# Performance work log

Hardware: AMD Instinct MI355X
Metric: run time of the kernel (lower is better)

## Reference

```python
import jax, jax.numpy as jnp
import numpy as np

S = 128           # seq_len
B = 256           # input_bits (bits per token, also neurons per head)
H = 16            # num_heads
NB = 12           # n_bits_per_neuron -> LUT size 2^12
PB = 7            # relative-position bits = ceil(log2(max_seq_len))
HEAD_IN = 2 * B + PB   # concat(query, key, rel_pos_bits) = 519
THRESH = H // 2


def setup_inputs() -> dict:
    key = jax.random.key(0)
    k1, k2, k3 = jax.random.split(key, 3)
    tokens = jax.random.randint(k1, (S, B), 0, 2, dtype=jnp.int32)           # binary token bits
    memory = jax.random.normal(k2, (H, B, 2 ** NB), dtype=jnp.float32)       # RAM LUT contents per head/neuron
    connections = jax.random.randint(k3, (H, B, NB), 0, HEAD_IN, dtype=jnp.int32)  # per-neuron input-bit wiring
    return {"tokens": tokens, "memory": memory, "connections": connections}


def reference(tokens, memory, connections):
    idx = jnp.arange(S)
    rel = idx[:, None] - idx[None, :]                         # [S,S] i - j
    mask = (rel >= 0).astype(jnp.int32)                        # causal mask (j <= i)
    relc = jnp.clip(rel, 0, S - 1)
    # relative-distance binary encoding, LSB first: [S,S,PB]
    pos_bits = ((relc[..., None] >> jnp.arange(PB)) & 1).astype(jnp.int32)
    q = jnp.broadcast_to(tokens[:, None, :], (S, S, B))
    k = jnp.broadcast_to(tokens[None, :, :], (S, S, B))
    head_in = jnp.concatenate([q, k, pos_bits], axis=-1)       # [S,S,HEAD_IN]
    # RAM address per (query i, key j, head h, neuron n): pack NB wired bits, LSB first
    addr = jnp.zeros((S, S, H, B), dtype=jnp.int32)
    for b in range(NB):  # tiny fixed loop over bit planes, fully vectorized over S,S,H,B
        addr = addr + (head_in[..., connections[:, :, b]] << b)
    # LUT gather: memory[h, n, addr] -> [S,S,H,B]
    h_idx = jnp.arange(H)[:, None]
    n_idx = jnp.arange(B)[None, :]
    vals = memory[h_idx, n_idx, addr]
    bits = (vals > 0.0).astype(jnp.int32)                      # RAM neuron output bit
    # XOR accumulation over attended keys == masked sum mod 2: [S,H,B]
    head_res = jnp.sum(bits * mask[:, :, None, None], axis=1) % 2
    # majority vote across heads per bit
    ones_count = jnp.sum(head_res, axis=1)                     # [S,B]
    return (ones_count > THRESH).astype(jnp.int32)
```

## Files before the change

### kernel.cpp

```cpp
#include <hip/hip_runtime.h>


#define S 128
#define B 256
#define H 16
#define NB 12

__device__ __forceinline__ unsigned sig(unsigned x) {
    return x ^ ((x >> 3) & 0x70u) ^ ((x >> 6) & 0x70u);
}

__global__ __launch_bounds__(1024, 4) void softram_kernel(
    const int* __restrict__ tokens,
    const float* __restrict__ memory,
    const int* __restrict__ connections,
    int* __restrict__ out)
{
    const int n    = blockIdx.x;
    const int tid  = threadIdx.x;
    const int h    = tid >> 6;
    const int lane = tid & 63;

    __shared__ unsigned char  bytetab[H * 4096];
    __shared__ unsigned int   tokT[8][S];
    __shared__ unsigned short akT[H][S];
    __shared__ unsigned short apt[H][S];
    __shared__ int            conns[H][NB];
    __shared__ unsigned int   parts[H][4];

    const float4* mrow = (const float4*)(memory + ((size_t)(h * 256 + n) << 12));
    float4 va[16];
    #pragma unroll
    for (int t = 0; t < 16; ++t) va[t] = mrow[lane + 64 * t];

    {
        int i = tid >> 3, w = tid & 7;
        const int4* tp = (const int4*)tokens;
        unsigned v = 0;
        #pragma unroll
        for (int u = 0; u < 8; ++u) {
            int4 x = tp[i * 64 + w * 8 + u];
            v |= (unsigned)(x.x & 1) << (4 * u + 0);
            v |= (unsigned)(x.y & 1) << (4 * u + 1);
            v |= (unsigned)(x.z & 1) << (4 * u + 2);
            v |= (unsigned)(x.w & 1) << (4 * u + 3);
        }
        tokT[w][i] = v;
    }
    if (tid < H * NB) {
        int hh = tid / NB, b = tid - hh * NB;
        conns[hh][b] = connections[hh * (B * NB) + n * NB + b];
    }
    __syncthreads();

    unsigned qmask = 0, kmask = 0, pmask = 0;
    #pragma unroll
    for (int b = 0; b < NB; ++b) {
        int c = conns[h][b];
        qmask |= (unsigned)(c < 256) << b;
        kmask |= (unsigned)(c >= 256 && c < 512) << b;
        pmask |= (unsigned)(c >= 512) << b;
    }
    const int qb = __popc(qmask);
    const int kb = __popc(kmask);

    unsigned char* __restrict__ bt = &bytetab[h << 12];
    unsigned long long rlo = 0, rhi = 0;

    if (pmask == 0) {
        unsigned qcls0 = 0, qcls1 = 0;
        #pragma unroll
        for (int e = 0; e < 2; ++e) {
            int ii = lane + 64 * e;
            unsigned qc = 0, kc = 0;
            int qn = 0, kn = 0;
            #pragma unroll
            for (int b = 0; b < NB; ++b) {
                int c = conns[h][b];
                if (c < 256) {
                    qc |= ((tokT[c >> 5][ii] >> (c & 31)) & 1u) << qn;
                    ++qn;
                } else {
                    int c2 = c - 256;
                    kc |= ((tokT[c2 >> 5][ii] >> (c2 & 31)) & 1u) << kn;
                    ++kn;
                }
            }
            akT[h][ii] = (unsigned short)kc;
            if (e == 0) qcls0 = qc; else qcls1 = qc;
        }

        #pragma unroll
        for (int t = 0; t < 16; ++t) {
            float4 v = va[t];
            unsigned p = 4u * (unsigned)(lane + 64 * t);
            unsigned w = (unsigned)(v.x > 0.f)
                       | ((unsigned)(v.y > 0.f) << 8)
                       | ((unsigned)(v.z > 0.f) << 16)
                       | ((unsigned)(v.w > 0.f) << 24);
            *(unsigned*)&bt[sig(p)] = w;
        }

        const bool formA = (qb <= 6);
        const int SBITS  = formA ? qb : kb;
        unsigned apl = 0, aul = 0;
        {
            int scnt = 0, lcnt = 0;
            #pragma unroll
            for (int b = 0; b < NB; ++b) {
                int c = conns[h][b];
                bool isS = formA ? (c < 256) : (c >= 256);
                if (isS) {
                    apl |= (((unsigned)lane >> scnt) & 1u) << b;
                    ++scnt;
                } else {
                    int p = SBITS + lcnt;
                    if (p < 6) apl |= (((unsigned)lane >> p) & 1u) << b;
                    else       aul |= (((unsigned)lane >> (p - 6)) & 1u) << b;
                    ++lcnt;
                }
            }
        }
        const unsigned spl  = sig(apl);
        const unsigned saul = sig(aul);
        unsigned Wlo = 0, Whi = 0;
        #pragma unroll 8
        for (int it = 0; it < 64; ++it) {
            unsigned sau  = (unsigned)__builtin_amdgcn_readlane((int)saul, it);
            unsigned bitv = bt[sau ^ spl] & 1u;
            unsigned long long Bm = __ballot(bitv != 0u);
            Wlo = (lane == it) ? (unsigned)Bm : Wlo;
            Whi = (lane == it) ? (unsigned)(Bm >> 32) : Whi;
        }

        if (formA) {
            unsigned long long A = 0, cap0 = 0, cap1 = 0;
            for (int s8 = 0; s8 < 8; ++s8) {
                uint4 uk = *(const uint4*)&akT[h][s8 * 8];
                #pragma unroll
                for (int t = 0; t < 8; ++t) {
                    int j = s8 * 8 + t;
                    unsigned w = ((const unsigned*)&uk)[t >> 1];
                    unsigned widx = (unsigned)__builtin_amdgcn_readfirstlane(
                        (int)((w >> ((t & 1) * 16)) & 0xffffu));
                    unsigned g0 = widx << qb;
                    int lsel = (int)(g0 >> 6);
                    unsigned lo = (unsigned)__builtin_amdgcn_readlane((int)Wlo, lsel);
                    unsigned hi = (unsigned)__builtin_amdgcn_readlane((int)Whi, lsel);
                    A ^= ((((unsigned long long)hi << 32) | lo) >> (g0 & 63u));
                    cap0 = (lane == j) ? A : cap0;
                }
            }
            for (int s8 = 8; s8 < 16; ++s8) {
                uint4 uk = *(const uint4*)&akT[h][s8 * 8];
                #pragma unroll
                for (int t = 0; t < 8; ++t) {
                    int j = s8 * 8 + t;
                    unsigned w = ((const unsigned*)&uk)[t >> 1];
                    unsigned widx = (unsigned)__builtin_amdgcn_readfirstlane(
                        (int)((w >> ((t & 1) * 16)) & 0xffffu));
                    unsigned g0 = widx << qb;
                    int lsel = (int)(g0 >> 6);
                    unsigned lo = (unsigned)__builtin_amdgcn_readlane((int)Wlo, lsel);
                    unsigned hi = (unsigned)__builtin_amdgcn_readlane((int)Whi, lsel);
                    A ^= ((((unsigned long long)hi << 32) | lo) >> (g0 & 63u));
                    cap1 = (lane == j - 64) ? A : cap1;
                }
            }
            rlo = __ballot(((cap0 >> qcls0) & 1ull) != 0ull);
            rhi = __ballot(((cap1 >> qcls1) & 1ull) != 0ull);
        } else {
            unsigned Cw = 0, cap0 = 0, cap1 = 0;
            for (int s8 = 0; s8 < 8; ++s8) {
                uint4 uk = *(const uint4*)&akT[h][s8 * 8];
                #pragma unroll
                for (int t = 0; t < 8; ++t) {
                    int j = s8 * 8 + t;
                    unsigned w = ((const unsigned*)&uk)[t >> 1];
                    unsigned widx = (unsigned)__builtin_amdgcn_readfirstlane(
                        (int)((w >> ((t & 1) * 16)) & 0xffffu));
                    Cw ^= 1u << widx;
                    cap0 = (lane == j) ? Cw : cap0;
                }
            }
            for (int s8 = 8; s8 < 16; ++s8) {
                uint4 uk = *(const uint4*)&akT[h][s8 * 8];
                #pragma unroll
                for (int t = 0; t < 8; ++t) {
                    int j = s8 * 8 + t;
                    unsigned w = ((const unsigned*)&uk)[t >> 1];
                    unsigned widx = (unsigned)__builtin_amdgcn_readfirstlane(
                        (int)((w >> ((t & 1) * 16)) & 0xffffu));
                    Cw ^= 1u << widx;
                    cap1 = (lane == j - 64) ? Cw : cap1;
                }
            }
            unsigned g0a = qcls0 << kb, g0b = qcls1 << kb;
            unsigned lo0 = (unsigned)__shfl((int)Wlo, (int)(g0a >> 6));
            unsigned hi0 = (unsigned)__shfl((int)Whi, (int)(g0a >> 6));
            unsigned lo1 = (unsigned)__shfl((int)Wlo, (int)(g0b >> 6));
            unsigned hi1 = (unsigned)__shfl((int)Whi, (int)(g0b >> 6));
            unsigned W0 = (unsigned)((((unsigned long long)hi0 << 32) | lo0) >> (g0a & 63u));
            unsigned W1 = (unsigned)((((unsigned long long)hi1 << 32) | lo1) >> (g0b & 63u));
            rlo = __ballot((__popc(W0 & cap0) & 1) != 0);
            rhi = __ballot((__popc(W1 & cap1) & 1) != 0);
        }
    } else {
        unsigned aqv0 = 0, aqv1 = 0;
        #pragma unroll
        for (int e = 0; e < 2; ++e) {
            int ii = lane + 64 * e;
            unsigned aq = 0, ak = 0, ap = 0;
            #pragma unroll
            for (int b = 0; b < NB; ++b) {
                int c = conns[h][b];
                if (c < 256) {
                    aq |= ((tokT[c >> 5][ii] >> (c & 31)) & 1u) << b;
                } else if (c < 512) {
                    int c2 = c - 256;
                    ak |= ((tokT[c2 >> 5][ii] >> (c2 & 31)) & 1u) << b;
                } else {
                    ap |= (((unsigned)ii >> (c - 512)) & 1u) << b;
                }
            }
            akT[h][ii] = (unsigned short)sig(ak);
            apt[h][ii] = (unsigned short)sig(ap);
            if (e == 0) aqv0 = sig(aq); else aqv1 = sig(aq);
        }

        #pragma unroll
        for (int t = 0; t < 16; ++t) {
            float4 v = va[t];
            unsigned p = 4u * (unsigned)(lane + 64 * t);
            unsigned w = (unsigned)(v.x > 0.f)
                       | ((unsigned)(v.y > 0.f) << 8)
                       | ((unsigned)(v.z > 0.f) << 16)
                       | ((unsigned)(v.w > 0.f) << 24);
            *(unsigned*)&bt[sig(p)] = w;
        }

        unsigned acc0 = 0, acc1 = 0;
        for (int s8 = 0; s8 < 8; ++s8) {
            uint4 uk = *(const uint4*)&akT[h][s8 * 8];
            #pragma unroll
            for (int t = 0; t < 8; ++t) {
                int j = s8 * 8 + t;
                unsigned w = ((const unsigned*)&uk)[t >> 1];
                unsigned akv = (w >> ((t & 1) * 16)) & 0xffffu;
                int d0 = lane - j;
                unsigned v0 = bt[aqv0 ^ akv ^ (unsigned)apt[h][d0 & 127]] & 1u;
                acc0 ^= (d0 >= 0) ? v0 : 0u;
                int d1 = lane + 64 - j;
                unsigned v1 = bt[aqv1 ^ akv ^ (unsigned)apt[h][d1]] & 1u;
                acc1 ^= v1;
            }
        }
        for (int s8 = 8; s8 < 16; ++s8) {
            uint4 uk = *(const uint4*)&akT[h][s8 * 8];
            #pragma unroll
            for (int t = 0; t < 8; ++t) {
                int j = s8 * 8 + t;
                unsigned w = ((const unsigned*)&uk)[t >> 1];
                unsigned akv = (w >> ((t & 1) * 16)) & 0xffffu;
                int d1 = lane + 64 - j;
                unsigned v1 = bt[aqv1 ^ akv ^ (unsigned)apt[h][d1 & 127]] & 1u;
                acc1 ^= (d1 >= 0) ? v1 : 0u;
            }
        }
        rlo = __ballot(acc0 != 0u);
        rhi = __ballot(acc1 != 0u);
    }

    if (lane == 0) {
        parts[h][0] = (unsigned)rlo;
        parts[h][1] = (unsigned)(rlo >> 32);
        parts[h][2] = (unsigned)rhi;
        parts[h][3] = (unsigned)(rhi >> 32);
    }
    __syncthreads();

    if (tid < S) {
        int i = tid, tot = 0;
        #pragma unroll
        for (int hh = 0; hh < H; ++hh)
            tot += (parts[hh][i >> 5] >> (i & 31)) & 1;
        out[i * B + n] = (tot > (H / 2)) ? 1 : 0;
    }
}

extern "C" void kernel_launch(void* const* d_in, const int* in_sizes, int n_in,
                              void* d_out, int out_size, void* d_ws, size_t ws_size,
                              hipStream_t stream) {
    const int*   tokens      = (const int*)d_in[0];
    const float* memory      = (const float*)d_in[1];
    const int*   connections = (const int*)d_in[2];
    int*         out         = (int*)d_out;
    (void)in_sizes; (void)n_in; (void)out_size; (void)d_ws; (void)ws_size;

    softram_kernel<<<B, 1024, 0, stream>>>(tokens, memory, connections, out);
}
```

Measured before the change: 117.0 us.

## Split heads across four blocks per neuron and add separate vote kernel

Each block now handles 4 heads (256 threads) instead of all 16 (1024 threads), giving 1024 blocks instead of 256. The per-block head counts go to a workspace buffer, and a second small kernel sums them and applies the majority threshold. The aim is better occupancy and load balance across CUs by using smaller blocks and less shared memory per block. In exchange, each block repeats the token bit-packing (four times the redundant work overall), and the extra launch plus workspace round trip adds overhead.

New measurement: 121.8 us. +4.1%, slower.

```diff
diff --git a/kernel.cpp b/kernel.cpp
--- a/kernel.cpp
+++ b/kernel.cpp
@@ -10,53 +10,60 @@
     return x ^ ((x >> 3) & 0x70u) ^ ((x >> 6) & 0x70u);
 }
 
-__global__ __launch_bounds__(1024, 4) void softram_kernel(
+__global__ __launch_bounds__(256, 4) void softram_kernel(
     const int* __restrict__ tokens,
     const float* __restrict__ memory,
     const int* __restrict__ connections,
-    int* __restrict__ out)
+    unsigned char* __restrict__ pc)
 {
-    const int n    = blockIdx.x;
+    const int bid  = blockIdx.x;
+    const int g    = bid >> 8;
+    const int n    = bid & 255;
     const int tid  = threadIdx.x;
-    const int h    = tid >> 6;
+    const int wid  = tid >> 6;
+    const int hg   = g * 4 + wid;
     const int lane = tid & 63;
 
-    __shared__ unsigned char  bytetab[H * 4096];
+    __shared__ unsigned char  bytetab[4 * 4096];
     __shared__ unsigned int   tokT[8][S];
-    __shared__ unsigned short akT[H][S];
-    __shared__ unsigned short apt[H][S];
-    __shared__ int            conns[H][NB];
-    __shared__ unsigned int   parts[H][4];
-
-    const float4* mrow = (const float4*)(memory + ((size_t)(h * 256 + n) << 12));
+    __shared__ unsigned short akT[4][S];
+    __shared__ unsigned short apt[4][S];
+    __shared__ int            conns[4][NB];
+    __shared__ unsigned int   parts[4][4];
+
+    const float4* mrow = (const float4*)(memory + ((size_t)(hg * 256 + n) << 12));
     float4 va[16];
     #pragma unroll
     for (int t = 0; t < 16; ++t) va[t] = mrow[lane + 64 * t];
 
     {
-        int i = tid >> 3, w = tid & 7;
+        int i = tid >> 1, half = tid & 1;
         const int4* tp = (const int4*)tokens;
-        unsigned v = 0;
-        #pragma unroll
-        for (int u = 0; u < 8; ++u) {
-            int4 x = tp[i * 64 + w * 8 + u];
-            v |= (unsigned)(x.x & 1) << (4 * u + 0);
-            v |= (unsigned)(x.y & 1) << (4 * u + 1);
-            v |= (unsigned)(x.z & 1) << (4 * u + 2);
-            v |= (unsigned)(x.w & 1) << (4 * u + 3);
-        }
-        tokT[w][i] = v;
-    }
-    if (tid < H * NB) {
+        #pragma unroll
+        for (int wl = 0; wl < 4; ++wl) {
+            int w = half * 4 + wl;
+            unsigned v = 0;
+            #pragma unroll
+            for (int u = 0; u < 8; ++u) {
+                int4 x = tp[i * 64 + w * 8 + u];
+                v |= (unsigned)(x.x & 1) << (4 * u + 0);
+                v |= (unsigned)(x.y & 1) << (4 * u + 1);
+                v |= (unsigned)(x.z & 1) << (4 * u + 2);
+                v |= (unsigned)(x.w & 1) << (4 * u + 3);
+            }
+            tokT[w][i] = v;
+        }
+    }
+    if (tid < 4 * NB) {
         int hh = tid / NB, b = tid - hh * NB;
-        conns[hh][b] = connections[hh * (B * NB) + n * NB + b];
+        conns[hh][b] = connections[(size_t)(g * 4 + hh) * (B * NB) + n * NB + b];
     }
     __syncthreads();
 
     unsigned qmask = 0, kmask = 0, pmask = 0;
     #pragma unroll
     for (int b = 0; b < NB; ++b) {
-        int c = conns[h][b];
+        int c = conns[wid][b];
         qmask |= (unsigned)(c < 256) << b;
         kmask |= (unsigned)(c >= 256 && c < 512) << b;
         pmask |= (unsigned)(c >= 512) << b;
@@ -64,7 +71,7 @@
     const int qb = __popc(qmask);
     const int kb = __popc(kmask);
 
-    unsigned char* __restrict__ bt = &bytetab[h << 12];
+    unsigned char* __restrict__ bt = &bytetab[wid << 12];
     unsigned long long rlo = 0, rhi = 0;
 
     if (pmask == 0) {
@@ -76,7 +83,7 @@
             int qn = 0, kn = 0;
             #pragma unroll
             for (int b = 0; b < NB; ++b) {
-                int c = conns[h][b];
+                int c = conns[wid][b];
                 if (c < 256) {
                     qc |= ((tokT[c >> 5][ii] >> (c & 31)) & 1u) << qn;
                     ++qn;
@@ -86,7 +93,7 @@
                     ++kn;
                 }
             }
-            akT[h][ii] = (unsigned short)kc;
+            akT[wid][ii] = (unsigned short)kc;
             if (e == 0) qcls0 = qc; else qcls1 = qc;
         }
 
@@ -108,7 +115,7 @@
             int scnt = 0, lcnt = 0;
             #pragma unroll
             for (int b = 0; b < NB; ++b) {
-                int c = conns[h][b];
+                int c = conns[wid][b];
                 bool isS = formA ? (c < 256) : (c >= 256);
                 if (isS) {
                     apl |= (((unsigned)lane >> scnt) & 1u) << b;
@@ -136,7 +143,7 @@
         if (formA) {
             unsigned long long A = 0, cap0 = 0, cap1 = 0;
             for (int s8 = 0; s8 < 8; ++s8) {
-                uint4 uk = *(const uint4*)&akT[h][s8 * 8];
+                uint4 uk = *(const uint4*)&akT[wid][s8 * 8];
                 #pragma unroll
                 for (int t = 0; t < 8; ++t) {
                     int j = s8 * 8 + t;
@@ -152,7 +159,7 @@
                 }
             }
             for (int s8 = 8; s8 < 16; ++s8) {
-                uint4 uk = *(const uint4*)&akT[h][s8 * 8];
+                uint4 uk = *(const uint4*)&akT[wid][s8 * 8];
                 #pragma unroll
                 for (int t = 0; t < 8; ++t) {
                     int j = s8 * 8 + t;
@@ -172,7 +179,7 @@
         } else {
             unsigned Cw = 0, cap0 = 0, cap1 = 0;
             for (int s8 = 0; s8 < 8; ++s8) {
-                uint4 uk = *(const uint4*)&akT[h][s8 * 8];
+                uint4 uk = *(const uint4*)&akT[wid][s8 * 8];
                 #pragma unroll
                 for (int t = 0; t < 8; ++t) {
                     int j = s8 * 8 + t;
@@ -184,7 +191,7 @@
                 }
             }
             for (int s8 = 8; s8 < 16; ++s8) {
-                uint4 uk = *(const uint4*)&akT[h][s8 * 8];
+                uint4 uk = *(const uint4*)&akT[wid][s8 * 8];
                 #pragma unroll
                 for (int t = 0; t < 8; ++t) {
                     int j = s8 * 8 + t;
@@ -213,7 +220,7 @@
             unsigned aq = 0, ak = 0, ap = 0;
             #pragma unroll
             for (int b = 0; b < NB; ++b) {
-                int c = conns[h][b];
+                int c = conns[wid][b];
                 if (c < 256) {
                     aq |= ((tokT[c >> 5][ii] >> (c & 31)) & 1u) << b;
                 } else if (c < 512) {
@@ -223,8 +230,8 @@
                     ap |= (((unsigned)ii >> (c - 512)) & 1u) << b;
                 }
             }
-            akT[h][ii] = (unsigned short)sig(ak);
-            apt[h][ii] = (unsigned short)sig(ap);
+            akT[wid][ii] = (unsigned short)sig(ak);
+            apt[wid][ii] = (unsigned short)sig(ap);
             if (e == 0) aqv0 = sig(aq); else aqv1 = sig(aq);
         }
 
@@ -241,29 +248,29 @@
 
         unsigned acc0 = 0, acc1 = 0;
         for (int s8 = 0; s8 < 8; ++s8) {
-            uint4 uk = *(const uint4*)&akT[h][s8 * 8];
+            uint4 uk = *(const uint4*)&akT[wid][s8 * 8];
             #pragma unroll
             for (int t = 0; t < 8; ++t) {
                 int j = s8 * 8 + t;
                 unsigned w = ((const unsigned*)&uk)[t >> 1];
                 unsigned akv = (w >> ((t & 1) * 16)) & 0xffffu;
                 int d0 = lane - j;
-                unsigned v0 = bt[aqv0 ^ akv ^ (unsigned)apt[h][d0 & 127]] & 1u;
+                unsigned v0 = bt[aqv0 ^ akv ^ (unsigned)apt[wid][d0 & 127]] & 1u;
                 acc0 ^= (d0 >= 0) ? v0 : 0u;
                 int d1 = lane + 64 - j;
-                unsigned v1 = bt[aqv1 ^ akv ^ (unsigned)apt[h][d1]] & 1u;
+                unsigned v1 = bt[aqv1 ^ akv ^ (unsigned)apt[wid][d1]] & 1u;
                 acc1 ^= v1;
             }
         }
         for (int s8 = 8; s8 < 16; ++s8) {
-            uint4 uk = *(const uint4*)&akT[h][s8 * 8];
+            uint4 uk = *(const uint4*)&akT[wid][s8 * 8];
             #pragma unroll
             for (int t = 0; t < 8; ++t) {
                 int j = s8 * 8 + t;
                 unsigned w = ((const unsigned*)&uk)[t >> 1];
                 unsigned akv = (w >> ((t & 1) * 16)) & 0xffffu;
                 int d1 = lane + 64 - j;
-                unsigned v1 = bt[aqv1 ^ akv ^ (unsigned)apt[h][d1 & 127]] & 1u;
+                unsigned v1 = bt[aqv1 ^ akv ^ (unsigned)apt[wid][d1 & 127]] & 1u;
                 acc1 ^= (d1 >= 0) ? v1 : 0u;
             }
         }
@@ -272,20 +279,33 @@
     }
 
     if (lane == 0) {
-        parts[h][0] = (unsigned)rlo;
-        parts[h][1] = (unsigned)(rlo >> 32);
-        parts[h][2] = (unsigned)rhi;
-        parts[h][3] = (unsigned)(rhi >> 32);
+        parts[wid][0] = (unsigned)rlo;
+        parts[wid][1] = (unsigned)(rlo >> 32);
+        parts[wid][2] = (unsigned)rhi;
+        parts[wid][3] = (unsigned)(rhi >> 32);
     }
     __syncthreads();
 
     if (tid < S) {
         int i = tid, tot = 0;
         #pragma unroll
-        for (int hh = 0; hh < H; ++hh)
+        for (int hh = 0; hh < 4; ++hh)
             tot += (parts[hh][i >> 5] >> (i & 31)) & 1;
-        out[i * B + n] = (tot > (H / 2)) ? 1 : 0;
-    }
+        pc[((size_t)g * 256 + n) * 128 + i] = (unsigned char)tot;
+    }
+}
+
+__global__ __launch_bounds__(128) void vote_kernel(
+    const unsigned char* __restrict__ pc,
+    int* __restrict__ out)
+{
+    const int n = blockIdx.x;
+    const int i = threadIdx.x;
+    int tot = pc[(size_t)(0 * 256 + n) * 128 + i]
+            + pc[(size_t)(1 * 256 + n) * 128 + i]
+            + pc[(size_t)(2 * 256 + n) * 128 + i]
+            + pc[(size_t)(3 * 256 + n) * 128 + i];
+    out[i * B + n] = (tot > (H / 2)) ? 1 : 0;
 }
 
 extern "C" void kernel_launch(void* const* d_in, const int* in_sizes, int n_in,
@@ -295,7 +315,9 @@
     const float* memory      = (const float*)d_in[1];
     const int*   connections = (const int*)d_in[2];
     int*         out         = (int*)d_out;
-    (void)in_sizes; (void)n_in; (void)out_size; (void)d_ws; (void)ws_size;
-
-    softram_kernel<<<B, 1024, 0, stream>>>(tokens, memory, connections, out);
+    unsigned char* pc        = (unsigned char*)d_ws;
+    (void)in_sizes; (void)n_in; (void)out_size; (void)ws_size;
+
+    softram_kernel<<<4 * B, 256, 0, stream>>>(tokens, memory, connections, pc);
+    vote_kernel<<<B, 128, 0, stream>>>(pc, out);
 }
```
